# Performance work log

Hardware: AMD Instinct MI355X
Metric: run time of the kernel (lower is better)

Reference implementation:

```python
import jax, jax.numpy as jnp
import numpy as np
from jax import lax

SIGMAS = (15.0, 80.0, 250.0)
DETAIL_WEIGHT = 0.0
ILLUM_WEIGHT = 1.0
EPS = 0.001


def _gaussian_kernel1d(sigma: float) -> np.ndarray:
    ks = int(2 * round(3 * sigma) + 1)
    if ks % 2 == 0:
        ks += 1
    x = np.arange(ks, dtype=np.float32) - (ks - 1) / 2.0
    k = np.exp(-0.5 * (x / sigma) ** 2)
    return (k / k.sum()).astype(np.float32)


def _gaussian_blur(img: jnp.ndarray, sigma: float) -> jnp.ndarray:
    # Separable Gaussian blur with reflect padding (kornia gaussian_blur2d semantics).
    k = jnp.asarray(_gaussian_kernel1d(sigma))
    ks = k.shape[0]
    p = ks // 2
    C = img.shape[1]
    dn = ('NCHW', 'OIHW', 'NCHW')
    kv = jnp.broadcast_to(k.reshape(1, 1, ks, 1), (C, 1, ks, 1))  # vertical pass
    kh = jnp.broadcast_to(k.reshape(1, 1, 1, ks), (C, 1, 1, ks))  # horizontal pass
    x = jnp.pad(img, ((0, 0), (0, 0), (p, p), (0, 0)), mode='reflect')
    x = lax.conv_general_dilated(x, kv, (1, 1), 'VALID', dimension_numbers=dn,
                                 feature_group_count=C)
    x = jnp.pad(x, ((0, 0), (0, 0), (0, 0), (p, p)), mode='reflect')
    x = lax.conv_general_dilated(x, kh, (1, 1), 'VALID', dimension_numbers=dn,
                                 feature_group_count=C)
    return x


def _multi_scale_retinex(input_img: jnp.ndarray) -> jnp.ndarray:
    img = jnp.clip(input_img, EPS, 1.0)
    log_img = jnp.log(img)
    acc = jnp.zeros_like(log_img)
    for sigma in SIGMAS:
        blur = jnp.maximum(_gaussian_blur(img, sigma), EPS)
        acc = acc + (log_img - jnp.log(blur))
    return acc / len(SIGMAS)


def setup_inputs() -> dict:
    key = jax.random.key(0)
    input_img = jax.random.uniform(key, (2, 3, 1024, 1024), dtype=jnp.float32)
    return {"input_img": input_img}


def reference(input_img):
    reflectance = _multi_scale_retinex(input_img)
    gx = reflectance[:, :, :, :-1] - reflectance[:, :, :, 1:]
    gy = reflectance[:, :, :-1, :] - reflectance[:, :, 1:, :]
    loss_detail = jnp.abs(gx).mean() + jnp.abs(gy).mean()
    illumination = jnp.log(jnp.maximum(input_img, EPS)) - reflectance
    igx = illumination[:, :, :, :-1] - illumination[:, :, :, 1:]
    igy = illumination[:, :, :-1, :] - illumination[:, :, 1:, :]
    loss_smooth_illum = jnp.abs(igx).mean() + jnp.abs(igy).mean()
    loss = DETAIL_WEIGHT * loss_detail + ILLUM_WEIGHT * loss_smooth_illum
    return (loss, loss_detail, loss_smooth_illum, reflectance, illumination)
```

## Files before the change

### kernel.cpp

```cpp
#include <hip/hip_runtime.h>
#include <math.h>

#define IMN 1024
#define IMGSZ (IMN * IMN)
#define NIMG 6
#define EPSV 0.001f
#define LDK 40
#define NB1 4096

typedef unsigned short u16;
typedef __attribute__((ext_vector_type(8))) short short8;
typedef __attribute__((ext_vector_type(16))) float floatx16;

__device__ __forceinline__ u16 rne_bf16(float v) {
  unsigned u = __float_as_uint(v);
  u = u + 0x7FFFu + ((u >> 16) & 1u);
  return (u16)(u >> 16);
}

__global__ __launch_bounds__(256) void build_taps_k(float* __restrict__ taps) {
  const int kss[3] = {91, 481, 1501};
  const float sig[3] = {15.f, 80.f, 250.f};
  int s = blockIdx.x;
  int ks = kss[s];
  float sigma = sig[s];
  float* t = taps + s * 1536;
  float ctr = (float)(ks - 1) * 0.5f;
  __shared__ float red[256];
  float loc = 0.f;
  for (int i = threadIdx.x; i < ks; i += 256) {
    float x = ((float)i - ctr) / sigma;
    float v = expf(-0.5f * x * x);
    t[i] = v;
    loc += v;
  }
  red[threadIdx.x] = loc;
  __syncthreads();
  for (int o = 128; o > 0; o >>= 1) {
    if (threadIdx.x < o) red[threadIdx.x] += red[threadIdx.x + o];
    __syncthreads();
  }
  float inv = 1.f / red[0];
  for (int i = threadIdx.x; i < ks; i += 256) t[i] *= inv;
}

__global__ __launch_bounds__(256) void build_w_k(const float* __restrict__ taps, int ks,
                                                 u16* __restrict__ WHr, u16* __restrict__ WLr) {
  int r = blockIdx.x;
  int p = ks >> 1;
  __shared__ float row[IMN];
  for (int i = threadIdx.x; i < IMN; i += 256) row[i] = 0.f;
  __syncthreads();
  for (int t = threadIdx.x; t < ks; t += 256) {
    int q = r + t - p;
    int j = q < 0 ? -q : (q > IMN - 1 ? 2 * (IMN - 1) - q : q);
    atomicAdd(&row[j], taps[t]);
  }
  __syncthreads();
  for (int i = threadIdx.x; i < IMN; i += 256) {
    float v = row[i];
    u16 h = rne_bf16(v);
    float hf = __uint_as_float((unsigned)h << 16);
    WHr[r * IMN + i] = h;
    WLr[r * IMN + i] = rne_bf16(v - hf);
  }
}

__global__ __launch_bounds__(256) void split_img_k(const float* __restrict__ inp,
                                                   u16* __restrict__ H) {
  int i4 = (blockIdx.x * 256 + threadIdx.x) * 4;
  float4 v = *(const float4*)&inp[i4];
  float x[4] = {v.x, v.y, v.z, v.w};
  u16 h[4];
#pragma unroll
  for (int e = 0; e < 4; e++) h[e] = rne_bf16(fminf(fmaxf(x[e], EPSV), 1.f));
  *(uint2*)&H[i4] = make_uint2((unsigned)h[0] | ((unsigned)h[1] << 16),
                               (unsigned)h[2] | ((unsigned)h[3] << 16));
}

template <int EPI>
__global__ __launch_bounds__(256, 4) void gemm_pass(
    const u16* __restrict__ AH, const u16* __restrict__ WH, const u16* __restrict__ WL,
    u16* __restrict__ OH, float* __restrict__ OF, int sBase, int outByZ, int rmw) {
  __shared__ u16 smem[3 * 128 * LDK];
  u16* Ah = smem;
  u16* Bh = smem + 128 * LDK;
  u16* Bl = smem + 2 * 128 * LDK;
  int z = blockIdx.z;
  int zs = z / 6;
  int s = (gridDim.z >= 18) ? (sBase + 2 - zs) : (sBase + zs);
  int i = z - zs * 6;
  const u16* Ag = AH + (size_t)(EPI == 0 ? i : z) * IMGSZ;
  const u16* BgH = WH + (size_t)s * IMGSZ;
  const u16* BgL = WL + (size_t)s * IMGSZ;
  int bm = blockIdx.y * 128, bn = blockIdx.x * 128;
  int tid = threadIdx.x;
  int lane = tid & 63, w = tid >> 6;
  int wm = (w >> 1) * 64, wn = (w & 1) * 64;
  int lrow = lane & 31, lh = lane >> 5;
  int tr = tid >> 2, tc = (tid & 3) * 8;
  floatx16 acc[2][2] = {};

  int p = (s == 0) ? 45 : (s == 1) ? 240 : 750;
  int klo = bn - p;
  klo = (klo < 0 ? 0 : klo) & ~31;
  int khi = bn + 128 + p;
  if (khi > IMN) khi = IMN;

  for (int k0 = klo; k0 < khi; k0 += 32) {
    uint4 a0 = *(const uint4*)&Ag[(size_t)(bm + tr) * IMN + k0 + tc];
    uint4 a1 = *(const uint4*)&Ag[(size_t)(bm + tr + 64) * IMN + k0 + tc];
    uint4 b0h = *(const uint4*)&BgH[(size_t)(bn + tr) * IMN + k0 + tc];
    uint4 b1h = *(const uint4*)&BgH[(size_t)(bn + tr + 64) * IMN + k0 + tc];
    uint4 b0l = *(const uint4*)&BgL[(size_t)(bn + tr) * IMN + k0 + tc];
    uint4 b1l = *(const uint4*)&BgL[(size_t)(bn + tr + 64) * IMN + k0 + tc];
    *(uint4*)&Ah[tr * LDK + tc] = a0;
    *(uint4*)&Ah[(tr + 64) * LDK + tc] = a1;
    *(uint4*)&Bh[tr * LDK + tc] = b0h;
    *(uint4*)&Bh[(tr + 64) * LDK + tc] = b1h;
    *(uint4*)&Bl[tr * LDK + tc] = b0l;
    *(uint4*)&Bl[(tr + 64) * LDK + tc] = b1l;
    __syncthreads();
#pragma unroll
    for (int kk = 0; kk < 32; kk += 16) {
      short8 ah[2], bh[2], bl[2];
#pragma unroll
      for (int mt = 0; mt < 2; mt++)
        ah[mt] = *(const short8*)&Ah[(wm + mt * 32 + lrow) * LDK + kk + lh * 8];
#pragma unroll
      for (int nt = 0; nt < 2; nt++) {
        int off = (wn + nt * 32 + lrow) * LDK + kk + lh * 8;
        bh[nt] = *(const short8*)&Bh[off];
        bl[nt] = *(const short8*)&Bl[off];
      }
#pragma unroll
      for (int mt = 0; mt < 2; mt++)
#pragma unroll
        for (int nt = 0; nt < 2; nt++) {
          acc[mt][nt] = __builtin_amdgcn_mfma_f32_32x32x16_bf16(ah[mt], bh[nt], acc[mt][nt], 0, 0, 0);
          acc[mt][nt] = __builtin_amdgcn_mfma_f32_32x32x16_bf16(ah[mt], bl[nt], acc[mt][nt], 0, 0, 0);
        }
    }
    __syncthreads();
  }

  float* lf = (float*)smem + w * 1056;
#pragma unroll
  for (int mt = 0; mt < 2; mt++)
#pragma unroll
    for (int nt = 0; nt < 2; nt++) {
#pragma unroll
      for (int rq = 0; rq < 4; rq++)
#pragma unroll
        for (int e = 0; e < 4; e++)
          lf[lrow * 33 + rq * 8 + lh * 4 + e] = acc[mt][nt][rq * 4 + e];
      __syncthreads();
#pragma unroll
      for (int p4 = 0; p4 < 4; p4++) {
        int rl = p4 * 8 + (lane >> 3);
        int cl = (lane & 7) * 4;
        float v0 = lf[rl * 33 + cl + 0];
        float v1 = lf[rl * 33 + cl + 1];
        float v2 = lf[rl * 33 + cl + 2];
        float v3 = lf[rl * 33 + cl + 3];
        int gn = bn + wn + nt * 32 + rl;
        int gm = bm + wm + mt * 32 + cl;
        if (EPI == 0) {
          size_t go = (size_t)z * IMGSZ + (size_t)gn * IMN + gm;
          *(uint2*)&OH[go] = make_uint2(
              (unsigned)rne_bf16(v0) | ((unsigned)rne_bf16(v1) << 16),
              (unsigned)rne_bf16(v2) | ((unsigned)rne_bf16(v3) << 16));
        } else {
          size_t go = (size_t)(outByZ ? z : i) * IMGSZ + (size_t)gn * IMN + gm;
          float4 rr = make_float4(logf(fmaxf(v0, EPSV)), logf(fmaxf(v1, EPSV)),
                                  logf(fmaxf(v2, EPSV)), logf(fmaxf(v3, EPSV)));
          if (rmw) {
            float4 pa = *(const float4*)&OF[go];
            rr.x += pa.x; rr.y += pa.y; rr.z += pa.z; rr.w += pa.w;
          }
          *(float4*)&OF[go] = rr;
        }
      }
      __syncthreads();
    }
}

__global__ __launch_bounds__(256) void loss_stage1_k(const float* __restrict__ inp,
                                                     const float* __restrict__ lb, int three,
                                                     float* __restrict__ refl,
                                                     float* __restrict__ illum,
                                                     float* __restrict__ pd,
                                                     float* __restrict__ ps) {
  const int stride = NB1 * 256;
  const int S = NIMG * IMGSZ;
  float sd = 0.f, ss = 0.f;
  for (int i = blockIdx.x * 256 + threadIdx.x; i < S; i += stride) {
    int c = i & (IMN - 1);
    int rr = (i >> 10) & (IMN - 1);
    float a0 = lb[i];
    if (three) a0 += lb[i + S] + lb[i + 2 * S];
    float I0 = a0 * (1.f / 3.f);
    float R0 = logf(fmaxf(inp[i], EPSV)) - I0;
    refl[i] = R0;
    illum[i] = I0;
    if (c < IMN - 1) {
      float a1 = lb[i + 1];
      if (three) a1 += lb[i + 1 + S] + lb[i + 1 + 2 * S];
      float I1 = a1 * (1.f / 3.f);
      float R1 = logf(fmaxf(inp[i + 1], EPSV)) - I1;
      sd += fabsf(R0 - R1);
      ss += fabsf(I0 - I1);
    }
    if (rr < IMN - 1) {
      float a2 = lb[i + IMN];
      if (three) a2 += lb[i + IMN + S] + lb[i + IMN + 2 * S];
      float I2 = a2 * (1.f / 3.f);
      float R2 = logf(fmaxf(inp[i + IMN], EPSV)) - I2;
      sd += fabsf(R0 - R2);
      ss += fabsf(I0 - I2);
    }
  }
  for (int o = 32; o > 0; o >>= 1) {
    sd += __shfl_down(sd, o);
    ss += __shfl_down(ss, o);
  }
  __shared__ float rsd[4], rss[4];
  int lane = threadIdx.x & 63, w = threadIdx.x >> 6;
  if (lane == 0) { rsd[w] = sd; rss[w] = ss; }
  __syncthreads();
  if (threadIdx.x == 0) {
    pd[blockIdx.x] = rsd[0] + rsd[1] + rsd[2] + rsd[3];
    ps[blockIdx.x] = rss[0] + rss[1] + rss[2] + rss[3];
  }
}

__global__ __launch_bounds__(256) void loss_stage2_k(const float* __restrict__ pd,
                                                     const float* __restrict__ ps,
                                                     float* __restrict__ out) {
  float sd = 0.f, ss = 0.f;
  for (int i = threadIdx.x; i < NB1; i += 256) {
    sd += pd[i];
    ss += ps[i];
  }
  for (int o = 32; o > 0; o >>= 1) {
    sd += __shfl_down(sd, o);
    ss += __shfl_down(ss, o);
  }
  __shared__ float rsd[4], rss[4];
  int lane = threadIdx.x & 63, w = threadIdx.x >> 6;
  if (lane == 0) { rsd[w] = sd; rss[w] = ss; }
  __syncthreads();
  if (threadIdx.x == 0) {
    float tsd = rsd[0] + rsd[1] + rsd[2] + rsd[3];
    float tss = rss[0] + rss[1] + rss[2] + rss[3];
    const float sc = 1.f / 6285312.f;
    out[0] = tss * sc;
    out[1] = tsd * sc;
    out[2] = tss * sc;
  }
}

extern "C" void kernel_launch(void* const* d_in, const int* in_sizes, int n_in,
                              void* d_out, int out_size, void* d_ws, size_t ws_size,
                              hipStream_t stream) {
  const float* inp = (const float*)d_in[0];
  float* out = (float*)d_out;
  float* refl = out + 3;
  float* illum = refl + (size_t)NIMG * IMGSZ;
  const int kss[3] = {91, 481, 1501};

  char* p = (char*)d_ws;
  float* taps = (float*)p;                  p += 32768;
  u16* WH = (u16*)p;                        p += (size_t)3 * IMGSZ * 2;
  u16* WL = (u16*)p;                        p += (size_t)3 * IMGSZ * 2;
  u16* imgH = (u16*)p;                      p += (size_t)NIMG * IMGSZ * 2;
  size_t fixed = (size_t)(p - (char*)d_ws);
  size_t needT1 = fixed + (size_t)18 * IMGSZ * 2 + (size_t)18 * IMGSZ * 4;
  bool t1 = ws_size >= needT1;
  int nz = t1 ? 18 : 6;
  u16* UtH = (u16*)p;                       p += (size_t)nz * IMGSZ * 2;
  float* LB = (float*)p;
  float* pd = taps;
  float* ps = taps + NB1;

  build_taps_k<<<3, 256, 0, stream>>>(taps);
  for (int s = 0; s < 3; s++)
    build_w_k<<<IMN, 256, 0, stream>>>(taps + s * 1536, kss[s],
                                       WH + (size_t)s * IMGSZ, WL + (size_t)s * IMGSZ);
  split_img_k<<<NIMG * IMGSZ / 1024, 256, 0, stream>>>(inp, imgH);

  if (t1) {
    dim3 g(8, 8, 18);
    gemm_pass<0><<<g, 256, 0, stream>>>(imgH, WH, WL, UtH, nullptr, 0, 1, 0);
    gemm_pass<1><<<g, 256, 0, stream>>>(UtH, WH, WL, nullptr, LB, 0, 1, 0);
  } else {
    dim3 g(8, 8, 6);
    for (int s = 0; s < 3; s++) {
      gemm_pass<0><<<g, 256, 0, stream>>>(imgH, WH, WL, UtH, nullptr, s, 0, 0);
      gemm_pass<1><<<g, 256, 0, stream>>>(UtH, WH, WL, nullptr, LB, s, 0, s > 0);
    }
  }
  loss_stage1_k<<<NB1, 256, 0, stream>>>(inp, LB, t1 ? 1 : 0, refl, illum, pd, ps);
  loss_stage2_k<<<1, 256, 0, stream>>>(pd, ps, out);
}
```

Measured before the change: 254.3 us.

## Double-buffer GEMM tiles with direct global-to-LDS loads and XOR swizzle

Replaces the register-staged global→LDS copy in the banded GEMM pass with direct global_load_lds 16-byte transfers into a double-buffered shared-memory tile, prefetching the next K tile while MFMAs consume the current one. The padded LDK=40 layout becomes an unpadded 32-wide layout with an XOR swizzle to avoid bank conflicts. This targets load latency and VGPR traffic in the main loop. In exchange LDS use doubles, which may reduce occupancy, and correctness depends on the swizzle and load mapping matching.

```diff
diff --git a/kernel.cpp b/kernel.cpp
--- a/kernel.cpp
+++ b/kernel.cpp
@@ -5,17 +5,22 @@
 #define IMGSZ (IMN * IMN)
 #define NIMG 6
 #define EPSV 0.001f
-#define LDK 40
 #define NB1 4096
 
 typedef unsigned short u16;
 typedef __attribute__((ext_vector_type(8))) short short8;
 typedef __attribute__((ext_vector_type(16))) float floatx16;
+typedef __attribute__((address_space(1))) const unsigned gu32;
+typedef __attribute__((address_space(3))) unsigned lu32;
 
 __device__ __forceinline__ u16 rne_bf16(float v) {
   unsigned u = __float_as_uint(v);
   u = u + 0x7FFFu + ((u >> 16) & 1u);
   return (u16)(u >> 16);
+}
+
+__device__ __forceinline__ void gl_lds16(const u16* g, u16* l) {
+  __builtin_amdgcn_global_load_lds((gu32*)g, (lu32*)l, 16, 0, 0);
 }
 
 __global__ __launch_bounds__(256) void build_taps_k(float* __restrict__ taps) {
@@ -82,10 +87,7 @@
 __global__ __launch_bounds__(256, 4) void gemm_pass(
     const u16* __restrict__ AH, const u16* __restrict__ WH, const u16* __restrict__ WL,
     u16* __restrict__ OH, float* __restrict__ OF, int sBase, int outByZ, int rmw) {
-  __shared__ u16 smem[3 * 128 * LDK];
-  u16* Ah = smem;
-  u16* Bh = smem + 128 * LDK;
-  u16* Bl = smem + 2 * 128 * LDK;
+  __shared__ u16 smem[2 * 3 * 128 * 32];
   int z = blockIdx.z;
   int zs = z / 6;
   int s = (gridDim.z >= 18) ? (sBase + 2 - zs) : (sBase + zs);
@@ -98,47 +100,65 @@
   int lane = tid & 63, w = tid >> 6;
   int wm = (w >> 1) * 64, wn = (w & 1) * 64;
   int lrow = lane & 31, lh = lane >> 5;
-  int tr = tid >> 2, tc = (tid & 3) * 8;
+  int sig = (lrow >> 1) & 3;
   floatx16 acc[2][2] = {};
+
+  int rl16 = lane >> 2;
+  int csw = ((lane & 3) ^ ((lane >> 3) & 3)) * 8;
+  const u16* gb[6];
+  int loff[6];
+#pragma unroll
+  for (int j = 0; j < 6; j++) {
+    int c = w * 6 + j;
+    int mat = c >> 3, sub = c & 7;
+    const u16* base = mat == 0 ? Ag : (mat == 1 ? BgH : BgL);
+    int row = (mat == 0 ? bm : bn) + sub * 16 + rl16;
+    gb[j] = base + (size_t)row * IMN + csw;
+    loff[j] = mat * 4096 + sub * 512;
+  }
 
   int p = (s == 0) ? 45 : (s == 1) ? 240 : 750;
   int klo = bn - p;
   klo = (klo < 0 ? 0 : klo) & ~31;
   int khi = bn + 128 + p;
   if (khi > IMN) khi = IMN;
-
-  for (int k0 = klo; k0 < khi; k0 += 32) {
-    uint4 a0 = *(const uint4*)&Ag[(size_t)(bm + tr) * IMN + k0 + tc];
-    uint4 a1 = *(const uint4*)&Ag[(size_t)(bm + tr + 64) * IMN + k0 + tc];
-    uint4 b0h = *(const uint4*)&BgH[(size_t)(bn + tr) * IMN + k0 + tc];
-    uint4 b1h = *(const uint4*)&BgH[(size_t)(bn + tr + 64) * IMN + k0 + tc];
-    uint4 b0l = *(const uint4*)&BgL[(size_t)(bn + tr) * IMN + k0 + tc];
-    uint4 b1l = *(const uint4*)&BgL[(size_t)(bn + tr + 64) * IMN + k0 + tc];
-    *(uint4*)&Ah[tr * LDK + tc] = a0;
-    *(uint4*)&Ah[(tr + 64) * LDK + tc] = a1;
-    *(uint4*)&Bh[tr * LDK + tc] = b0h;
-    *(uint4*)&Bh[(tr + 64) * LDK + tc] = b1h;
-    *(uint4*)&Bl[tr * LDK + tc] = b0l;
-    *(uint4*)&Bl[(tr + 64) * LDK + tc] = b1l;
-    __syncthreads();
+  int ktiles = (khi - klo + 31) >> 5;
+
+#pragma unroll
+  for (int j = 0; j < 6; j++) gl_lds16(gb[j] + klo, &smem[loff[j]]);
+  __syncthreads();
+
+  for (int t = 0; t < ktiles; t++) {
+    if (t + 1 < ktiles) {
+      u16* lb = &smem[((t + 1) & 1) * 12288];
+      int k1 = klo + (t + 1) * 32;
+#pragma unroll
+      for (int j = 0; j < 6; j++) gl_lds16(gb[j] + k1, &lb[loff[j]]);
+    }
+    const u16* S = &smem[(t & 1) * 12288];
 #pragma unroll
     for (int kk = 0; kk < 32; kk += 16) {
+      int sl = (kk >> 3) + lh;
+      int so = ((sl ^ sig) * 8);
       short8 ah[2], bh[2], bl[2];
 #pragma unroll
+      for (int mt = 0; mt < 2; mt++) {
+        int ra = wm + mt * 32 + lrow;
+        ah[mt] = *(const short8*)&S[ra * 32 + so];
+      }
+#pragma unroll
+      for (int nt2 = 0; nt2 < 2; nt2++) {
+        int rb = wn + nt2 * 32 + lrow;
+        int o = rb * 32 + so;
+        bh[nt2] = *(const short8*)&S[4096 + o];
+        bl[nt2] = *(const short8*)&S[8192 + o];
+      }
+#pragma unroll
       for (int mt = 0; mt < 2; mt++)
-        ah[mt] = *(const short8*)&Ah[(wm + mt * 32 + lrow) * LDK + kk + lh * 8];
-#pragma unroll
-      for (int nt = 0; nt < 2; nt++) {
-        int off = (wn + nt * 32 + lrow) * LDK + kk + lh * 8;
-        bh[nt] = *(const short8*)&Bh[off];
-        bl[nt] = *(const short8*)&Bl[off];
-      }
-#pragma unroll
-      for (int mt = 0; mt < 2; mt++)
-#pragma unroll
-        for (int nt = 0; nt < 2; nt++) {
-          acc[mt][nt] = __builtin_amdgcn_mfma_f32_32x32x16_bf16(ah[mt], bh[nt], acc[mt][nt], 0, 0, 0);
-          acc[mt][nt] = __builtin_amdgcn_mfma_f32_32x32x16_bf16(ah[mt], bl[nt], acc[mt][nt], 0, 0, 0);
+#pragma unroll
+        for (int nt2 = 0; nt2 < 2; nt2++) {
+          acc[mt][nt2] = __builtin_amdgcn_mfma_f32_32x32x16_bf16(ah[mt], bh[nt2], acc[mt][nt2], 0, 0, 0);
+          acc[mt][nt2] = __builtin_amdgcn_mfma_f32_32x32x16_bf16(ah[mt], bl[nt2], acc[mt][nt2], 0, 0, 0);
         }
     }
     __syncthreads();
```

After: 258.1 us. Within noise of the previous version (+1.5%).
